# Kernel optimization log

Measured on AMD Instinct MI355X. Metric: run time of the kernel, lower is better.

## Reference

```python
import jax, jax.numpy as jnp
import numpy as np

FP8_MAX = 448.0  # max representable magnitude of float8_e4m3fn


def _quantize_tensorwise(x):
    """Tensor-wise fp8 quantization. Returns (fp8 tensor, inverse_scale) where
    dequant = fp8.astype(f32) * inverse_scale (matches Fp8Quantization.quantize_tensorwise)."""
    amax = jnp.max(jnp.abs(x))
    inv_scale = jnp.maximum(amax / FP8_MAX, jnp.float32(1e-12))
    q = (x / inv_scale).astype(jnp.float8_e4m3fn)
    return q, inv_scale


def _fp8_mm(qa, qb, sa, sb):
    # scaled fp8 GEMM: accumulate in f32, apply product of per-tensor inverse scales
    return (qa.astype(jnp.float32) @ qb.astype(jnp.float32)) * (sa * sb)


def setup_inputs() -> dict:
    key = jax.random.key(0)
    k1, k2, k3 = jax.random.split(key, 3)
    x = jax.random.normal(k1, (4, 2048, 2048), dtype=jnp.float32)
    weight = jax.random.normal(k2, (2048, 2048), dtype=jnp.float32) * 0.02
    bias = jax.random.normal(k3, (2048,), dtype=jnp.float32) * 0.01
    return {"x": x, "weight": weight, "bias": bias}


def reference(x, weight, bias):
    # flatten leading dims: inputmat = input.view(-1, K)
    K = x.shape[-1]
    xm = x.reshape(-1, K)                      # [T, K]
    qx, sx = _quantize_tensorwise(xm)          # fp8 input + inverse scale
    qwt, swt = _quantize_tensorwise(weight.T)  # fp8 weight^T [K, N] + inverse scale
    out = _fp8_mm(qx, qwt, sx, swt) + bias     # [T, N]
    return out.reshape(*x.shape[:-1], -1)
```

## Files before the change

kernel.cpp:

```cpp
#include <hip/hip_runtime.h>
#include <stdint.h>

typedef float f32x4 __attribute__((ext_vector_type(4)));
typedef int   i32x4 __attribute__((ext_vector_type(4)));
typedef int   i32x8 __attribute__((ext_vector_type(8)));

__global__ __launch_bounds__(256) void amax2_kernel(
    const float* __restrict__ x, int nx4,
    const float* __restrict__ w, int nw4,
    int xblocks, int* __restrict__ out) {
  const float4* src;
  int n4, j0, stride, slot;
  if ((int)blockIdx.x < xblocks) {
    src = (const float4*)x; n4 = nx4; slot = 0;
    j0 = blockIdx.x * blockDim.x + threadIdx.x;
    stride = xblocks * blockDim.x;
  } else {
    src = (const float4*)w; n4 = nw4; slot = 1;
    j0 = (blockIdx.x - xblocks) * blockDim.x + threadIdx.x;
    stride = (gridDim.x - xblocks) * blockDim.x;
  }
  float m = 0.f;
  for (int j = j0; j < n4; j += stride) {
    float4 v = src[j];
    m = fmaxf(m, fmaxf(fmaxf(fabsf(v.x), fabsf(v.y)),
                       fmaxf(fabsf(v.z), fabsf(v.w))));
  }
#pragma unroll
  for (int off = 32; off; off >>= 1)
    m = fmaxf(m, __shfl_down(m, off, 64));
  __shared__ float red[4];
  const int lane = threadIdx.x & 63;
  const int wv = threadIdx.x >> 6;
  if (lane == 0) red[wv] = m;
  __syncthreads();
  if (threadIdx.x == 0) {
    m = fmaxf(fmaxf(red[0], red[1]), fmaxf(red[2], red[3]));
    atomicMax(out + slot, (int)__float_as_uint(m));
  }
}

__global__ __launch_bounds__(256) void quant2_kernel(
    const float* __restrict__ x, unsigned char* __restrict__ qx, int nx4,
    const float* __restrict__ w, unsigned char* __restrict__ qw, int nw4,
    int xblocks, const unsigned* __restrict__ amax2) {
  const float4* src;
  unsigned* dst;
  int n4, j0, stride;
  float amax;
  if ((int)blockIdx.x < xblocks) {
    src = (const float4*)x; dst = (unsigned*)qx; n4 = nx4;
    amax = __uint_as_float(amax2[0]);
    j0 = blockIdx.x * blockDim.x + threadIdx.x;
    stride = xblocks * blockDim.x;
  } else {
    src = (const float4*)w; dst = (unsigned*)qw; n4 = nw4;
    amax = __uint_as_float(amax2[1]);
    j0 = (blockIdx.x - xblocks) * blockDim.x + threadIdx.x;
    stride = (gridDim.x - xblocks) * blockDim.x;
  }
  const float inv_scale = fmaxf(amax / 448.0f, 1e-12f);
  for (int j = j0; j < n4; j += stride) {
    float4 v = src[j];
    float a0 = v.x / inv_scale;
    float a1 = v.y / inv_scale;
    float a2 = v.z / inv_scale;
    float a3 = v.w / inv_scale;
    int p = 0;
    p = __builtin_amdgcn_cvt_pk_fp8_f32(a0, a1, p, false);
    p = __builtin_amdgcn_cvt_pk_fp8_f32(a2, a3, p, true);
    dst[j] = (unsigned)p;
  }
}

#define BM 128
#define BN 128
#define BK 128

__device__ __forceinline__ void load_lds16(const void* g, void* l) {
  __builtin_amdgcn_global_load_lds(
      (const __attribute__((address_space(1))) unsigned int*)g,
      (__attribute__((address_space(3))) unsigned int*)l, 16, 0, 0);
}

__global__ __launch_bounds__(256) void gemm_fp8_kernel(
    const unsigned char* __restrict__ Aq,
    const unsigned char* __restrict__ Bq,
    const float* __restrict__ bias,
    const unsigned* __restrict__ amax2,
    float* __restrict__ out,
    int T, int N, int K) {
  __shared__ __align__(16) unsigned char sA[BM * BK];
  __shared__ __align__(16) unsigned char sB[BN * BK];

  const int tid = threadIdx.x;
  const int lane = tid & 63;
  const int wave = tid >> 6;
  const int wm = (wave >> 1) * 64;
  const int wn = (wave & 1) * 64;
  const long m0 = (long)blockIdx.y * BM;
  const long n0 = (long)blockIdx.x * BN;

  f32x4 acc[4][4];
#pragma unroll
  for (int i = 0; i < 4; i++)
#pragma unroll
    for (int j = 0; j < 4; j++) acc[i][j] = (f32x4){0.f, 0.f, 0.f, 0.f};

  const int row_s = tid >> 3;
  const int c_s = tid & 7;
  const int scol = (c_s ^ (row_s & 7)) << 4;
  const int o = tid * 16;
  const unsigned char* aSrc[4];
  const unsigned char* bSrc[4];
#pragma unroll
  for (int r = 0; r < 4; r++) {
    aSrc[r] = Aq + (m0 + r * 32 + row_s) * (long)K + scol;
    bSrc[r] = Bq + (n0 + r * 32 + row_s) * (long)K + scol;
  }

  const int lm = lane & 15;
  const int q = lane >> 4;
  const int kc0 = q * 2;
  const int sxr = lm & 7;

  for (int k0 = 0; k0 < K; k0 += BK) {
#pragma unroll
    for (int r = 0; r < 4; r++) {
      load_lds16(aSrc[r] + k0, sA + r * 4096 + o);
      load_lds16(bSrc[r] + k0, sB + r * 4096 + o);
    }
    __syncthreads();

    i32x8 af[4], bf[4];
    const int c0 = (kc0 ^ sxr) << 4;
    const int c1 = ((kc0 + 1) ^ sxr) << 4;
#pragma unroll
    for (int mt = 0; mt < 4; mt++) {
      const unsigned char* p = sA + (wm + mt * 16 + lm) * BK;
      i32x4 lo = *(const i32x4*)(p + c0);
      i32x4 hi = *(const i32x4*)(p + c1);
      af[mt] = (i32x8){lo.x, lo.y, lo.z, lo.w, hi.x, hi.y, hi.z, hi.w};
    }
#pragma unroll
    for (int nt = 0; nt < 4; nt++) {
      const unsigned char* p = sB + (wn + nt * 16 + lm) * BK;
      i32x4 lo = *(const i32x4*)(p + c0);
      i32x4 hi = *(const i32x4*)(p + c1);
      bf[nt] = (i32x8){lo.x, lo.y, lo.z, lo.w, hi.x, hi.y, hi.z, hi.w};
    }
#pragma unroll
    for (int mt = 0; mt < 4; mt++)
#pragma unroll
      for (int nt = 0; nt < 4; nt++)
        acc[mt][nt] = __builtin_amdgcn_mfma_scale_f32_16x16x128_f8f6f4(
            af[mt], bf[nt], acc[mt][nt],
             0,  0,
             0, 0x7f7f7f7f,  0, 0x7f7f7f7f);
    __syncthreads();
  }

  const float sx = fmaxf(__uint_as_float(amax2[0]) / 448.0f, 1e-12f);
  const float sw = fmaxf(__uint_as_float(amax2[1]) / 448.0f, 1e-12f);
  const float scale = sx * sw;
  const int rbase = (lane >> 4) * 4;
#pragma unroll
  for (int mt = 0; mt < 4; mt++) {
#pragma unroll
    for (int r = 0; r < 4; r++) {
      const long row = m0 + wm + mt * 16 + rbase + r;
      float* orow = out + row * (long)N + n0 + wn;
#pragma unroll
      for (int nt = 0; nt < 4; nt++) {
        const int col = nt * 16 + lm;
        orow[col] = acc[mt][nt][r] * scale + bias[n0 + wn + col];
      }
    }
  }
}

extern "C" void kernel_launch(void* const* d_in, const int* in_sizes, int n_in,
                              void* d_out, int out_size, void* d_ws, size_t ws_size,
                              hipStream_t stream) {
  const float* x = (const float*)d_in[0];
  const float* w = (const float*)d_in[1];
  const float* bias = (const float*)d_in[2];
  float* out = (float*)d_out;

  const int N = in_sizes[2];
  const int K = in_sizes[1] / N;
  const int T = in_sizes[0] / K;

  unsigned* amax2 = (unsigned*)d_ws;
  unsigned char* qx = (unsigned char*)d_ws + 256;
  unsigned char* qw = qx + (size_t)T * K;

  const int XB = 1024;
  const int WB = 256;
  amax2_kernel<<<XB + WB, 256, 0, stream>>>(x, T * K / 4, w, N * K / 4, XB,
                                            (int*)amax2);
  quant2_kernel<<<XB + WB, 256, 0, stream>>>(x, qx, T * K / 4, w, qw, N * K / 4,
                                             XB, amax2);

  dim3 grid(N / BN, T / BM);
  gemm_fp8_kernel<<<grid, 256, 0, stream>>>(qx, qw, bias, amax2, out, T, N, K);
}
```

Measured before the change: 189.8 us.

## Fuse amax and quantize via grid barrier; use 32x32 MFMA with 256-row tiles

Merges the amax and quantization kernels into one persistent-style kernel. Blocks sync through an atomic counter spin barrier, so one launch is saved and the second read can hit cache. The GEMM moves to 256x128 tiles with 32x32x64 scaled fp8 MFMA and occupancy hint 2, for more reuse per LDS load. The workspace is now zeroed explicitly with a memset. The spin barrier relies on all 1024 blocks being co-resident and risks deadlock if they are not.

```diff
diff --git a/kernel.cpp b/kernel.cpp
--- a/kernel.cpp
+++ b/kernel.cpp
@@ -1,25 +1,27 @@
 #include <hip/hip_runtime.h>
 #include <stdint.h>
 
-typedef float f32x4 __attribute__((ext_vector_type(4)));
+typedef float f32x16 __attribute__((ext_vector_type(16)));
 typedef int   i32x4 __attribute__((ext_vector_type(4)));
 typedef int   i32x8 __attribute__((ext_vector_type(8)));
 
-__global__ __launch_bounds__(256) void amax2_kernel(
-    const float* __restrict__ x, int nx4,
-    const float* __restrict__ w, int nw4,
-    int xblocks, int* __restrict__ out) {
+__global__ __launch_bounds__(256, 4) void amax_quant_kernel(
+    const float* __restrict__ x, unsigned char* __restrict__ qx, int nx4,
+    const float* __restrict__ w, unsigned char* __restrict__ qw, int nw4,
+    int xblocks, int nblocks, unsigned* __restrict__ sync) {
   const float4* src;
+  unsigned* dst;
   int n4, j0, stride, slot;
   if ((int)blockIdx.x < xblocks) {
-    src = (const float4*)x; n4 = nx4; slot = 0;
+    src = (const float4*)x; dst = (unsigned*)qx; n4 = nx4; slot = 0;
     j0 = blockIdx.x * blockDim.x + threadIdx.x;
     stride = xblocks * blockDim.x;
   } else {
-    src = (const float4*)w; n4 = nw4; slot = 1;
+    src = (const float4*)w; dst = (unsigned*)qw; n4 = nw4; slot = 1;
     j0 = (blockIdx.x - xblocks) * blockDim.x + threadIdx.x;
     stride = (gridDim.x - xblocks) * blockDim.x;
   }
+
   float m = 0.f;
   for (int j = j0; j < n4; j += stride) {
     float4 v = src[j];
@@ -34,31 +36,21 @@
   const int wv = threadIdx.x >> 6;
   if (lane == 0) red[wv] = m;
   __syncthreads();
+
   if (threadIdx.x == 0) {
     m = fmaxf(fmaxf(red[0], red[1]), fmaxf(red[2], red[3]));
-    atomicMax(out + slot, (int)__float_as_uint(m));
+    atomicMax(sync + slot, __float_as_uint(m));
+    __threadfence();
+    __hip_atomic_fetch_add(sync + 2, 1u, __ATOMIC_ACQ_REL,
+                           __HIP_MEMORY_SCOPE_AGENT);
+    while (__hip_atomic_load(sync + 2, __ATOMIC_ACQUIRE,
+                             __HIP_MEMORY_SCOPE_AGENT) < (unsigned)nblocks)
+      __builtin_amdgcn_s_sleep(8);
   }
-}
+  __syncthreads();
 
-__global__ __launch_bounds__(256) void quant2_kernel(
-    const float* __restrict__ x, unsigned char* __restrict__ qx, int nx4,
-    const float* __restrict__ w, unsigned char* __restrict__ qw, int nw4,
-    int xblocks, const unsigned* __restrict__ amax2) {
-  const float4* src;
-  unsigned* dst;
-  int n4, j0, stride;
-  float amax;
-  if ((int)blockIdx.x < xblocks) {
-    src = (const float4*)x; dst = (unsigned*)qx; n4 = nx4;
-    amax = __uint_as_float(amax2[0]);
-    j0 = blockIdx.x * blockDim.x + threadIdx.x;
-    stride = xblocks * blockDim.x;
-  } else {
-    src = (const float4*)w; dst = (unsigned*)qw; n4 = nw4;
-    amax = __uint_as_float(amax2[1]);
-    j0 = (blockIdx.x - xblocks) * blockDim.x + threadIdx.x;
-    stride = (gridDim.x - xblocks) * blockDim.x;
-  }
+  const float amax = __uint_as_float(__hip_atomic_load(
+      sync + slot, __ATOMIC_ACQUIRE, __HIP_MEMORY_SCOPE_AGENT));
   const float inv_scale = fmaxf(amax / 448.0f, 1e-12f);
   for (int j = j0; j < n4; j += stride) {
     float4 v = src[j];
@@ -73,7 +65,7 @@
   }
 }
 
-#define BM 128
+#define BM 256
 #define BN 128
 #define BK 128
 
@@ -83,7 +75,7 @@
       (__attribute__((address_space(3))) unsigned int*)l, 16, 0, 0);
 }
 
-__global__ __launch_bounds__(256) void gemm_fp8_kernel(
+__global__ __launch_bounds__(256, 2) void gemm_fp8_kernel(
     const unsigned char* __restrict__ Aq,
     const unsigned char* __restrict__ Bq,
     const float* __restrict__ bias,
@@ -96,85 +88,84 @@
   const int tid = threadIdx.x;
   const int lane = tid & 63;
   const int wave = tid >> 6;
-  const int wm = (wave >> 1) * 64;
+  const int wm = (wave >> 1) * 128;
   const int wn = (wave & 1) * 64;
   const long m0 = (long)blockIdx.y * BM;
   const long n0 = (long)blockIdx.x * BN;
 
-  f32x4 acc[4][4];
+  f32x16 acc[4][2];
 #pragma unroll
   for (int i = 0; i < 4; i++)
 #pragma unroll
-    for (int j = 0; j < 4; j++) acc[i][j] = (f32x4){0.f, 0.f, 0.f, 0.f};
+    for (int j = 0; j < 2; j++)
+#pragma unroll
+      for (int r = 0; r < 16; r++) acc[i][j][r] = 0.f;
 
   const int row_s = tid >> 3;
-  const int c_s = tid & 7;
-  const int scol = (c_s ^ (row_s & 7)) << 4;
+  const int scol = ((tid & 7) ^ (row_s & 7)) << 4;
   const int o = tid * 16;
-  const unsigned char* aSrc[4];
-  const unsigned char* bSrc[4];
-#pragma unroll
-  for (int r = 0; r < 4; r++) {
-    aSrc[r] = Aq + (m0 + r * 32 + row_s) * (long)K + scol;
-    bSrc[r] = Bq + (n0 + r * 32 + row_s) * (long)K + scol;
-  }
+  const unsigned char* aBase = Aq + (m0 + row_s) * (long)K + scol;
+  const unsigned char* bBase = Bq + (n0 + row_s) * (long)K + scol;
 
-  const int lm = lane & 15;
-  const int q = lane >> 4;
-  const int kc0 = q * 2;
-  const int sxr = lm & 7;
+  const int lr = lane & 31;
+  const int kh = lane >> 5;
+  const int swz = lr & 7;
 
   for (int k0 = 0; k0 < K; k0 += BK) {
 #pragma unroll
-    for (int r = 0; r < 4; r++) {
-      load_lds16(aSrc[r] + k0, sA + r * 4096 + o);
-      load_lds16(bSrc[r] + k0, sB + r * 4096 + o);
-    }
+    for (int r = 0; r < 8; r++)
+      load_lds16(aBase + (long)r * 32 * K + k0, sA + r * 4096 + o);
+#pragma unroll
+    for (int r = 0; r < 4; r++)
+      load_lds16(bBase + (long)r * 32 * K + k0, sB + r * 4096 + o);
     __syncthreads();
 
-    i32x8 af[4], bf[4];
-    const int c0 = (kc0 ^ sxr) << 4;
-    const int c1 = ((kc0 + 1) ^ sxr) << 4;
 #pragma unroll
-    for (int mt = 0; mt < 4; mt++) {
-      const unsigned char* p = sA + (wm + mt * 16 + lm) * BK;
-      i32x4 lo = *(const i32x4*)(p + c0);
-      i32x4 hi = *(const i32x4*)(p + c1);
-      af[mt] = (i32x8){lo.x, lo.y, lo.z, lo.w, hi.x, hi.y, hi.z, hi.w};
+    for (int s = 0; s < 2; s++) {
+      const int kc0 = s * 4 + kh * 2;
+      const int c0 = (kc0 ^ swz) << 4;
+      const int c1 = ((kc0 + 1) ^ swz) << 4;
+      i32x8 af[4], bf[2];
+#pragma unroll
+      for (int mt = 0; mt < 4; mt++) {
+        const unsigned char* p = sA + (wm + mt * 32 + lr) * BK;
+        i32x4 lo = *(const i32x4*)(p + c0);
+        i32x4 hi = *(const i32x4*)(p + c1);
+        af[mt] = (i32x8){lo.x, lo.y, lo.z, lo.w, hi.x, hi.y, hi.z, hi.w};
+      }
+#pragma unroll
+      for (int nt = 0; nt < 2; nt++) {
+        const unsigned char* p = sB + (wn + nt * 32 + lr) * BK;
+        i32x4 lo = *(const i32x4*)(p + c0);
+        i32x4 hi = *(const i32x4*)(p + c1);
+        bf[nt] = (i32x8){lo.x, lo.y, lo.z, lo.w, hi.x, hi.y, hi.z, hi.w};
+      }
+#pragma unroll
+      for (int mt = 0; mt < 4; mt++)
+#pragma unroll
+        for (int nt = 0; nt < 2; nt++)
+          acc[mt][nt] = __builtin_amdgcn_mfma_scale_f32_32x32x64_f8f6f4(
+              af[mt], bf[nt], acc[mt][nt],
+               0,  0,
+               0, 0x7f7f7f7f,  0, 0x7f7f7f7f);
     }
-#pragma unroll
-    for (int nt = 0; nt < 4; nt++) {
-      const unsigned char* p = sB + (wn + nt * 16 + lm) * BK;
-      i32x4 lo = *(const i32x4*)(p + c0);
-      i32x4 hi = *(const i32x4*)(p + c1);
-      bf[nt] = (i32x8){lo.x, lo.y, lo.z, lo.w, hi.x, hi.y, hi.z, hi.w};
-    }
-#pragma unroll
-    for (int mt = 0; mt < 4; mt++)
-#pragma unroll
-      for (int nt = 0; nt < 4; nt++)
-        acc[mt][nt] = __builtin_amdgcn_mfma_scale_f32_16x16x128_f8f6f4(
-            af[mt], bf[nt], acc[mt][nt],
-             0,  0,
-             0, 0x7f7f7f7f,  0, 0x7f7f7f7f);
     __syncthreads();
   }
 
   const float sx = fmaxf(__uint_as_float(amax2[0]) / 448.0f, 1e-12f);
   const float sw = fmaxf(__uint_as_float(amax2[1]) / 448.0f, 1e-12f);
   const float scale = sx * sw;
-  const int rbase = (lane >> 4) * 4;
+  const float bv0 = bias[n0 + wn + lr];
+  const float bv1 = bias[n0 + wn + 32 + lr];
 #pragma unroll
   for (int mt = 0; mt < 4; mt++) {
 #pragma unroll
-    for (int r = 0; r < 4; r++) {
-      const long row = m0 + wm + mt * 16 + rbase + r;
-      float* orow = out + row * (long)N + n0 + wn;
-#pragma unroll
-      for (int nt = 0; nt < 4; nt++) {
-        const int col = nt * 16 + lm;
-        orow[col] = acc[mt][nt][r] * scale + bias[n0 + wn + col];
-      }
+    for (int reg = 0; reg < 16; reg++) {
+      const long row =
+          m0 + wm + mt * 32 + (reg & 3) + 8 * (reg >> 2) + 4 * kh;
+      float* orow = out + row * (long)N + n0 + wn + lr;
+      orow[0] = acc[mt][0][reg] * scale + bv0;
+      orow[32] = acc[mt][1][reg] * scale + bv1;
     }
   }
 }
@@ -191,17 +182,17 @@
   const int K = in_sizes[1] / N;
   const int T = in_sizes[0] / K;
 
-  unsigned* amax2 = (unsigned*)d_ws;
+  unsigned* sync = (unsigned*)d_ws;
   unsigned char* qx = (unsigned char*)d_ws + 256;
   unsigned char* qw = qx + (size_t)T * K;
 
-  const int XB = 1024;
+  hipMemsetAsync(d_ws, 0, 256, stream);
+
+  const int XB = 768;
   const int WB = 256;
-  amax2_kernel<<<XB + WB, 256, 0, stream>>>(x, T * K / 4, w, N * K / 4, XB,
-                                            (int*)amax2);
-  quant2_kernel<<<XB + WB, 256, 0, stream>>>(x, qx, T * K / 4, w, qw, N * K / 4,
-                                             XB, amax2);
+  amax_quant_kernel<<<XB + WB, 256, 0, stream>>>(
+      x, qx, T * K / 4, w, qw, N * K / 4, XB, XB + WB, sync);
 
   dim3 grid(N / BN, T / BM);
-  gemm_fp8_kernel<<<grid, 256, 0, stream>>>(qx, qw, bias, amax2, out, T, N, K);
+  gemm_fp8_kernel<<<grid, 256, 0, stream>>>(qx, qw, bias, sync, out, T, N, K);
 }
```

New measurement: 320.5 us. 1.69x slower.
